# Optimization experiments

Measured on AMD Instinct MI355X. Metric: run time of the kernel, lower is better.

The kernel has to match this reference:

```python
import jax, jax.numpy as jnp
import numpy as np

N_ANCHORS = 262144
B = 4
G = 64
IM_SIZE = 1024.0
STRADDLE = 0.0
POS_THR = 0.5
NEG_THR = 0.3
FG_FRAC = 0.3
SAMPLE_BATCH = 512
TARGET_FG = int(FG_FRAC * SAMPLE_BATCH)  # 153
NEG_LOGIT = -1e9


def _jaccard(a, b):
    # Detectron-legacy '+1' box convention. a:[N,4], b:[G,4] -> [N,G]
    area_a = (a[:, 2] - a[:, 0] + 1.0) * (a[:, 3] - a[:, 1] + 1.0)
    area_b = (b[:, 2] - b[:, 0] + 1.0) * (b[:, 3] - b[:, 1] + 1.0)
    lt = jnp.maximum(a[:, None, :2], b[None, :, :2])
    rb = jnp.minimum(a[:, None, 2:], b[None, :, 2:])
    wh = jnp.clip(rb - lt + 1.0, 0.0)
    inter = wh[..., 0] * wh[..., 1]
    return inter / (area_a[:, None] + area_b[None, :] - inter)


def _bbox_transform_inv(ex, gt):
    ew = ex[:, 2] - ex[:, 0] + 1.0
    eh = ex[:, 3] - ex[:, 1] + 1.0
    ecx = ex[:, 0] + 0.5 * ew
    ecy = ex[:, 1] + 0.5 * eh
    gw = gt[:, 2] - gt[:, 0] + 1.0
    gh = gt[:, 3] - gt[:, 1] + 1.0
    gcx = gt[:, 0] + 0.5 * gw
    gcy = gt[:, 1] + 0.5 * gh
    return jnp.stack([(gcx - ecx) / ew, (gcy - ecy) / eh,
                      jnp.log(gw / ew), jnp.log(gh / eh)], axis=1)


def _match_single(boxes, gt_boxes, gt_ignore, im_info, key):
    # mask-based (jit-friendly) equivalent of forward_single_image; outside
    # anchors keep label -1 / targets 0, which reproduces the unmap() step.
    n = boxes.shape[0]
    im_h, im_w = im_info[0], im_info[1]
    inside = ((boxes[:, 0] >= -STRADDLE) & (boxes[:, 1] >= -STRADDLE)
              & (boxes[:, 2] < im_w + STRADDLE + 1.0)
              & (boxes[:, 3] < im_h + STRADDLE + 1.0))
    valid_gt = gt_ignore == 0  # gt_boxes[gt_ignore_labels == 0]
    iou = jnp.where(inside[:, None] & valid_gt[None, :], _jaccard(boxes, gt_boxes), 0.0)
    a2g_max = iou.max(axis=1)
    a2g_idx = iou.argmax(axis=1)
    g2a_max = iou.max(axis=0)
    g2a_max = jnp.where(g2a_max == 0.0, 1.0, g2a_max)  # avoid matching all-zero cols
    with_max = (iou == g2a_max[None, :]).any(axis=1)   # ensure_closest_box
    pos = inside & (with_max | (a2g_max >= POS_THR))
    labels = jnp.where(pos, 1, -1).astype(jnp.int32)
    # subsample positives down to TARGET_FG by random priority (keeps exactly
    # min(fg_num, TARGET_FG) positives, like the permutation-based disable)
    kp, kn = jax.random.split(key)
    prio = jnp.where(pos, jax.random.uniform(kp, (n,)), -jnp.inf)
    rank = jnp.argsort(jnp.argsort(-prio))
    labels = jnp.where(pos & (rank >= TARGET_FG), -1, labels)
    # sample negatives with replacement (torch.multinomial(..., replacement=True))
    num_fg = (labels > 0).sum()
    target_bg = SAMPLE_BATCH - num_fg
    neg = inside & (a2g_max < NEG_THR)
    do_sample = neg.sum() > target_bg
    samp = jax.random.categorical(kn, jnp.where(neg, 0.0, NEG_LOGIT), shape=(SAMPLE_BATCH,))
    valid_s = jnp.arange(SAMPLE_BATCH) < target_bg
    idx = jnp.where(valid_s, samp, n)  # invalid samples write to padded slot
    lab_ext = jnp.concatenate([labels, jnp.full((1,), -1, jnp.int32)])
    lab_samp = lab_ext.at[idx].set(0)[:n]
    labels = jnp.where(do_sample, lab_samp, labels)
    pos_final = labels > 0
    deltas = _bbox_transform_inv(boxes, gt_boxes[a2g_idx])
    bbox_targets = jnp.where(pos_final[:, None], deltas, 0.0)
    return labels, bbox_targets


def setup_inputs() -> dict:
    key = jax.random.key(0)
    k1, k2, k3, k4, k5, k6 = jax.random.split(key, 6)
    axy = jax.random.uniform(k1, (N_ANCHORS, 2), minval=-50.0, maxval=950.0)
    awh = jax.random.uniform(k2, (N_ANCHORS, 2), minval=16.0, maxval=160.0)
    boxes = jnp.concatenate([axy, axy + awh], axis=1)
    gxy = jax.random.uniform(k3, (B, G, 2), minval=0.0, maxval=800.0)
    gwh = jax.random.uniform(k4, (B, G, 2), minval=32.0, maxval=220.0)
    gt_boxes = jnp.concatenate([gxy, gxy + gwh], axis=2)
    gt_labels = jax.random.randint(k5, (B, G), 0, 80)
    gt_ignore_labels = jax.random.randint(k6, (B, G), 0, 2)
    im_info = jnp.tile(jnp.array([IM_SIZE, IM_SIZE, 1.0], jnp.float32), (B, 1))
    return {"boxes": boxes, "gt_boxes": gt_boxes, "gt_labels": gt_labels,
            "gt_ignore_labels": gt_ignore_labels, "im_info": im_info}


def reference(boxes, gt_boxes, gt_labels, gt_ignore_labels, im_info):
    # gt_labels is accepted but unused, exactly as in the torch module
    keys = jax.random.split(jax.random.key(42), gt_boxes.shape[0])
    labels, bbox_targets = jax.vmap(_match_single, in_axes=(None, 0, 0, 0, 0))(
        boxes.reshape(-1, 4), gt_boxes, gt_ignore_labels, im_info, keys)
    return labels, bbox_targets
```

## Files before the change

kernel.cpp:

```cpp
#include <hip/hip_runtime.h>
#include <stdint.h>

#define NANCH   262144
#define NB      4
#define NG      64
#define TGT_FG  153
#define SB      512
#define IDXMASK 262143u
#define NSH     8
#define SHCAP   (NANCH/NSH)

#define WS_PCNT     0
#define WS_G2A      4096
#define WS_KTH      5120
#define WS_TBG      5184
#define WS_DOSAMP   5248
#define WS_NUMPOS   5312
#define WS_SAMPKEY  8192
#define WS_ZERO_WORDS 6144
#define WS_A2G      32768
#define WS_NEG      (WS_A2G + NB*NANCH)
#define WS_POS      (WS_NEG + NB*NANCH*4)

#define PCNT_AT(pcnt, b, sh, L) ((pcnt)[(((b) * NSH + (sh)) * 2 + (L)) * 16])

struct RngKeys { uint32_t kp[NB][2]; uint32_t kn[NB][2]; };

#define TFR(r) { x0 += x1; x1 = (x1 << (r)) | (x1 >> (32 - (r))); x1 ^= x0; }
__host__ __device__ inline void tf2x32(uint32_t k0, uint32_t k1,
                                       uint32_t x0, uint32_t x1,
                                       uint32_t &o0, uint32_t &o1) {
  uint32_t k2 = k0 ^ k1 ^ 0x1BD11BDAu;
  x0 += k0; x1 += k1;
  TFR(13) TFR(15) TFR(26) TFR(6)   x0 += k1; x1 += k2 + 1u;
  TFR(17) TFR(29) TFR(16) TFR(24)  x0 += k2; x1 += k0 + 2u;
  TFR(13) TFR(15) TFR(26) TFR(6)   x0 += k0; x1 += k1 + 3u;
  TFR(17) TFR(29) TFR(16) TFR(24)  x0 += k1; x1 += k2 + 4u;
  TFR(13) TFR(15) TFR(26) TFR(6)   x0 += k2; x1 += k0 + 5u;
  o0 = x0; o1 = x1;
}

__host__ __device__ inline void tf_ctr(uint32_t k0, uint32_t k1, uint32_t i,
                                       uint32_t &o0, uint32_t &o1) {
  tf2x32(k0, k1, 0u, i, o0, o1);
}

__device__ __forceinline__ uint32_t draw_bits(uint32_t k0, uint32_t k1,
                                              uint32_t idx) {
  uint32_t o0, o1;
  tf_ctr(k0, k1, idx, o0, o1);
  return o0 ^ o1;
}

#define ROTL1(x, r) __builtin_amdgcn_alignbit((x), (x), 32 - (r))
#define TFQ(r) { x0 += x1; x1 = ROTL1(x1, r); x1 ^= x0; }
__device__ __forceinline__ uint32_t tf_bits_fast(uint32_t k0, uint32_t k1,
                                                 uint32_t k2, uint32_t x0,
                                                 uint32_t x1) {
  TFQ(13) TFQ(15) TFQ(26) TFQ(6)   x0 += k1; x1 += k2 + 1u;
  TFQ(17) TFQ(29) TFQ(16) TFQ(24)  x0 += k2; x1 += k0 + 2u;
  TFQ(13) TFQ(15) TFQ(26) TFQ(6)   x0 += k0; x1 += k1 + 3u;
  TFQ(17) TFQ(29) TFQ(16) TFQ(24)  x0 += k1; x1 += k2 + 4u;
  TFQ(13) TFQ(15) TFQ(26) TFQ(6)   x0 += k2; x1 += k0 + 5u;
  return x0 ^ x1;
}

__device__ __forceinline__ float box_area(float x1, float y1, float x2, float y2) {
#pragma clang fp contract(off)
  return ((x2 - x1) + 1.0f) * ((y2 - y1) + 1.0f);
}

__device__ __forceinline__ float iou_pair(float ax1, float ay1, float ax2, float ay2,
                                          float areaA, float gx1, float gy1,
                                          float gx2, float gy2, float areaB) {
#pragma clang fp contract(off)
  float ltx = fmaxf(ax1, gx1), lty = fmaxf(ay1, gy1);
  float rbx = fminf(ax2, gx2), rby = fminf(ay2, gy2);
  float w = fmaxf((rbx - ltx) + 1.0f, 0.0f);
  float h = fmaxf((rby - lty) + 1.0f, 0.0f);
  float inter = w * h;
  return inter / ((areaA + areaB) - inter);
}

__global__ __launch_bounds__(256) void k_init(unsigned int* w) {
  int i = blockIdx.x * 256 + threadIdx.x;
  if (i < WS_ZERO_WORDS) w[i] = 0u;
}

__global__ __launch_bounds__(256) void k_g2amax(
    const float4* __restrict__ boxes, const float4* __restrict__ gtb,
    const int* __restrict__ gti, const float* __restrict__ iminfo,
    unsigned int* __restrict__ g2a_u32) {
  int bx = blockIdx.x;
  int b = bx >> 8, chunk = bx & 255;
  int t = threadIdx.x, j = t & 63, sub = t >> 6;
  float4 g = gtb[b * NG + j];
  bool valid = (gti[b * NG + j] == 0);
  float areaB = box_area(g.x, g.y, g.z, g.w);
  float thrx = iminfo[b * 3 + 1] + 1.0f;
  float thry = iminfo[b * 3 + 0] + 1.0f;
  float m = 0.0f;
  int base = chunk * 1024 + sub * 256;
  #pragma unroll 2
  for (int i = 0; i < 256; ++i) {
    float4 bb = boxes[base + i];
    bool inside = (bb.x >= -0.0f) && (bb.y >= -0.0f) && (bb.z < thrx) && (bb.w < thry);
    float areaA = box_area(bb.x, bb.y, bb.z, bb.w);
    float v = iou_pair(bb.x, bb.y, bb.z, bb.w, areaA, g.x, g.y, g.z, g.w, areaB);
    v = (inside && valid) ? v : 0.0f;
    m = fmaxf(m, v);
  }
  __shared__ float red[4][64];
  red[sub][j] = m;
  __syncthreads();
  if (t < 64) {
    float mm = fmaxf(fmaxf(red[0][t], red[1][t]), fmaxf(red[2][t], red[3][t]));
    atomicMax(&g2a_u32[b * NG + t], __float_as_uint(mm));
  }
}

__global__ __launch_bounds__(256) void k_label(
    const float4* __restrict__ boxes, const float4* __restrict__ gtb,
    const int* __restrict__ gti, const float* __restrict__ iminfo,
    const float* __restrict__ g2a, float* __restrict__ labels,
    unsigned char* __restrict__ a2g, unsigned long long* __restrict__ pos_keys,
    unsigned int* __restrict__ neg_list, int* __restrict__ pcnt, RngKeys rk) {
  int bx = blockIdx.x;
  int b = bx >> 10, blk = bx & 1023;
  int t = threadIdx.x;
  int sh = blk & (NSH - 1);
  __shared__ float4 sg[NG];
  __shared__ float sab[NG], sval[NG], sadj[NG];
  if (t < NG) {
    float4 g = gtb[b * NG + t];
    sg[t] = g;
    sab[t] = box_area(g.x, g.y, g.z, g.w);
    sval[t] = (gti[b * NG + t] == 0) ? 1.0f : 0.0f;
    float gm = g2a[b * NG + t];
    sadj[t] = (gm == 0.0f) ? 1.0f : gm;
  }
  __syncthreads();
  int a = blk * 256 + t;
  float4 bb = boxes[a];
  float thrx = iminfo[b * 3 + 1] + 1.0f, thry = iminfo[b * 3 + 0] + 1.0f;
  bool inside = (bb.x >= -0.0f) && (bb.y >= -0.0f) && (bb.z < thrx) && (bb.w < thry);
  float areaA = box_area(bb.x, bb.y, bb.z, bb.w);
  float maxv = 0.0f; int amax = 0; bool wm = false;
  #pragma unroll 8
  for (int j = 0; j < NG; ++j) {
    float4 g = sg[j];
    float v = iou_pair(bb.x, bb.y, bb.z, bb.w, areaA, g.x, g.y, g.z, g.w, sab[j]);
    v = (inside && (sval[j] != 0.0f)) ? v : 0.0f;
    wm = wm || (v == sadj[j]);
    if (v > maxv) { maxv = v; amax = j; }
  }
  bool pos = inside && (wm || (maxv >= 0.5f));
  bool neg = inside && (maxv < 0.3f);
  labels[b * NANCH + a] = pos ? 1.0f : -1.0f;
  a2g[b * NANCH + a] = (unsigned char)amax;
  unsigned long long mpos = __ballot(pos);
  unsigned long long mneg = __ballot(neg);
  int lane = t & 63, wid = t >> 6;
  __shared__ int wc[4][2];
  __shared__ int bbase[2];
  if (lane == 0) { wc[wid][0] = __popcll(mpos); wc[wid][1] = __popcll(mneg); }
  __syncthreads();
  if (t == 0) {
    bbase[0] = atomicAdd(&PCNT_AT(pcnt, b, sh, 0),
                         wc[0][0] + wc[1][0] + wc[2][0] + wc[3][0]);
    bbase[1] = atomicAdd(&PCNT_AT(pcnt, b, sh, 1),
                         wc[0][1] + wc[1][1] + wc[2][1] + wc[3][1]);
  }
  __syncthreads();
  unsigned long long lt = (1ull << lane) - 1ull;
  if (pos) {
    int off = bbase[0] + __popcll(mpos & lt);
    for (int w = 0; w < wid; ++w) off += wc[w][0];
    uint32_t bits = draw_bits(rk.kp[b][0], rk.kp[b][1], (uint32_t)a);
    unsigned long long key =
        (((unsigned long long)(bits >> 9)) << 18) | (unsigned long long)(IDXMASK - (uint32_t)a);
    pos_keys[(size_t)b * NANCH + (size_t)sh * SHCAP + off] = key;
  }
  if (neg) {
    int off = bbase[1] + __popcll(mneg & lt);
    for (int w = 0; w < wid; ++w) off += wc[w][1];
    neg_list[(size_t)b * NANCH + (size_t)sh * SHCAP + off] = (unsigned int)a;
  }
}

__global__ __launch_bounds__(256) void k_select(
    const unsigned long long* __restrict__ pos_keys, const int* __restrict__ pcnt,
    unsigned long long* __restrict__ kth, int* __restrict__ tbg,
    int* __restrict__ dosamp, int* __restrict__ numpos) {
  int b = blockIdx.x, t = threadIdx.x;
  int scnt[NSH]; int np = 0, nn = 0;
  #pragma unroll
  for (int sh = 0; sh < NSH; ++sh) {
    scnt[sh] = PCNT_AT(pcnt, b, sh, 0);
    np += scnt[sh];
    nn += PCNT_AT(pcnt, b, sh, 1);
  }
  int nf = np < TGT_FG ? np : TGT_FG;
  int targ = SB - nf;
  if (t == 0) { tbg[b] = targ; dosamp[b] = (nn > targ) ? 1 : 0; numpos[b] = np; }
  if (np <= TGT_FG) { if (t == 0) kth[b] = 0ull; return; }
  __shared__ int cw[4];
  int lane = t & 63, wid = t >> 6;
  unsigned long long pref = 0ull;
  int r = TGT_FG;
  for (int bit = 40; bit >= 0; --bit) {
    unsigned long long cand = pref | (1ull << bit);
    unsigned long long mask = ~((1ull << bit) - 1ull);
    int c = 0;
    for (int sh = 0; sh < NSH; ++sh) {
      const unsigned long long* keys =
          pos_keys + (size_t)b * NANCH + (size_t)sh * SHCAP;
      for (int i = t; i < scnt[sh]; i += 256)
        c += ((keys[i] & mask) == cand) ? 1 : 0;
    }
    #pragma unroll
    for (int off = 32; off; off >>= 1) c += __shfl_xor(c, off, 64);
    __syncthreads();
    if (lane == 0) cw[wid] = c;
    __syncthreads();
    int total = cw[0] + cw[1] + cw[2] + cw[3];
    if (total >= r) pref = cand; else r -= total;
  }
  if (t == 0) kth[b] = pref;
}

__global__ __launch_bounds__(256) void k_disable(
    const unsigned long long* __restrict__ pos_keys, const int* __restrict__ pcnt,
    const int* __restrict__ numpos, const unsigned long long* __restrict__ kth,
    float* __restrict__ labels) {
  int b = blockIdx.x >> 6, blk = blockIdx.x & 63;
  if (numpos[b] <= TGT_FG) return;
  int sh = blk & (NSH - 1), sub = blk >> 3;
  int cnt = PCNT_AT(pcnt, b, sh, 0);
  unsigned long long K = kth[b];
  const unsigned long long* keys = pos_keys + (size_t)b * NANCH + (size_t)sh * SHCAP;
  for (int i = sub * 256 + threadIdx.x; i < cnt; i += 8 * 256) {
    unsigned long long key = keys[i];
    if (key < K) {
      int a = (int)(IDXMASK - (uint32_t)(key & (unsigned long long)IDXMASK));
      labels[b * NANCH + a] = -1.0f;
    }
  }
}

__global__ __launch_bounds__(256) void k_cat(
    const unsigned int* __restrict__ neg_list, const int* __restrict__ pcnt,
    const int* __restrict__ tbg, unsigned long long* __restrict__ samp_key,
    RngKeys rk) {
  int bx = blockIdx.x;
  int sh = bx & (NSH - 1);
  int pr = (bx >> 3) & 255;
  int b  = bx >> 11;
  int targ = tbg[b];
  int s0 = pr * 2;
  if (s0 >= targ) return;
  int nn = PCNT_AT(pcnt, b, sh, 1);
  uint32_t k0 = rk.kn[b][0], k1 = rk.kn[b][1];
  uint32_t k2 = k0 ^ k1 ^ 0x1BD11BDAu;
  uint32_t xb0 = ((uint32_t)s0 << 18) + k1;
  uint32_t xb1 = ((uint32_t)(s0 + 1) << 18) + k1;
  unsigned long long b0 = 0ull, b1 = 0ull;
  const unsigned int* nl = neg_list + (size_t)b * NANCH + (size_t)sh * SHCAP;
  int i = threadIdx.x;
  if (i < nn) {
    uint32_t a = nl[i];
    for (;;) {
      int inext = i + 256;
      bool has = inext < nn;
      uint32_t an = has ? nl[inext] : 0u;
      unsigned long long inv64 = (unsigned long long)(IDXMASK - a);
      { uint32_t bits = tf_bits_fast(k0, k1, k2, k0, xb0 + a);
        unsigned long long key = (((unsigned long long)(bits >> 9)) << 18) | inv64;
        if (key > b0) b0 = key; }
      { uint32_t bits = tf_bits_fast(k0, k1, k2, k0, xb1 + a);
        unsigned long long key = (((unsigned long long)(bits >> 9)) << 18) | inv64;
        if (key > b1) b1 = key; }
      if (!has) break;
      a = an; i = inext;
    }
  }
  #pragma unroll
  for (int off = 32; off; off >>= 1) {
    unsigned long long o0 = __shfl_xor(b0, off, 64); if (o0 > b0) b0 = o0;
    unsigned long long o1 = __shfl_xor(b1, off, 64); if (o1 > b1) b1 = o1;
  }
  __shared__ unsigned long long red[4][2];
  int lane = threadIdx.x & 63, wid = threadIdx.x >> 6;
  if (lane == 0) { red[wid][0] = b0; red[wid][1] = b1; }
  __syncthreads();
  if (threadIdx.x < 2) {
    int j = threadIdx.x;
    unsigned long long m = red[0][j];
    if (red[1][j] > m) m = red[1][j];
    if (red[2][j] > m) m = red[2][j];
    if (red[3][j] > m) m = red[3][j];
    if (s0 + j < targ) atomicMax(&samp_key[b * SB + s0 + j], m);
  }
}

__global__ __launch_bounds__(256) void k_scatter(
    const unsigned long long* __restrict__ samp_key, const int* __restrict__ tbg,
    const int* __restrict__ dosamp, float* __restrict__ labels) {
  int b = blockIdx.x >> 1;
  int s = ((blockIdx.x & 1) << 8) | threadIdx.x;
  if (!dosamp[b]) return;
  if (s < tbg[b]) {
    unsigned long long key = samp_key[b * SB + s];
    int a = (int)(IDXMASK - (uint32_t)(key & (unsigned long long)IDXMASK));
    labels[b * NANCH + a] = 0.0f;
  }
}

__global__ __launch_bounds__(256) void k_targets(
    const float4* __restrict__ boxes, const float4* __restrict__ gtb,
    const unsigned char* __restrict__ a2g, const float* __restrict__ labels,
    float4* __restrict__ tout) {
  int bx = blockIdx.x;
  int b = bx >> 10, blk = bx & 1023;
  int a = blk * 256 + threadIdx.x;
  float lab = labels[b * NANCH + a];
  float4 o = make_float4(0.f, 0.f, 0.f, 0.f);
  if (lab > 0.0f) {
    float4 e = boxes[a];
    float4 g = gtb[b * NG + a2g[b * NANCH + a]];
    float ew = e.z - e.x + 1.0f, eh = e.w - e.y + 1.0f;
    float ecx = e.x + 0.5f * ew, ecy = e.y + 0.5f * eh;
    float gw = g.z - g.x + 1.0f, gh = g.w - g.y + 1.0f;
    float gcx = g.x + 0.5f * gw, gcy = g.y + 0.5f * gh;
    o.x = (gcx - ecx) / ew;
    o.y = (gcy - ecy) / eh;
    o.z = logf(gw / ew);
    o.w = logf(gh / eh);
  }
  tout[(size_t)b * NANCH + a] = o;
}

extern "C" void kernel_launch(void* const* d_in, const int* in_sizes, int n_in,
                              void* d_out, int out_size, void* d_ws, size_t ws_size,
                              hipStream_t stream) {
  const float4* boxes  = (const float4*)d_in[0];
  const float4* gtb    = (const float4*)d_in[1];
  const int*    gti    = (const int*)d_in[3];
  const float*  iminfo = (const float*)d_in[4];
  float*  labels = (float*)d_out;
  float4* tout   = (float4*)(labels + (size_t)NB * NANCH);

  char* wsb = (char*)d_ws;
  int*                pcnt     = (int*)(wsb + WS_PCNT);
  unsigned int*       g2a_u32  = (unsigned int*)(wsb + WS_G2A);
  float*              g2a_f    = (float*)(wsb + WS_G2A);
  unsigned long long* kth      = (unsigned long long*)(wsb + WS_KTH);
  int*                tbg      = (int*)(wsb + WS_TBG);
  int*                dosamp   = (int*)(wsb + WS_DOSAMP);
  int*                numpos   = (int*)(wsb + WS_NUMPOS);
  unsigned long long* samp_key = (unsigned long long*)(wsb + WS_SAMPKEY);
  unsigned char*      a2g      = (unsigned char*)(wsb + WS_A2G);
  unsigned int*       neg_list = (unsigned int*)(wsb + WS_NEG);
  unsigned long long* pos_keys = (unsigned long long*)(wsb + WS_POS);

  RngKeys rk;
  for (int b = 0; b < NB; ++b) {
    uint32_t a0, a1;
    tf_ctr(0u, 42u, (uint32_t)b, a0, a1);
    tf_ctr(a0, a1, 0u, rk.kp[b][0], rk.kp[b][1]);
    tf_ctr(a0, a1, 1u, rk.kn[b][0], rk.kn[b][1]);
  }

  k_init   <<<24, 256, 0, stream>>>((unsigned int*)wsb);
  k_g2amax <<<NB * (NANCH / 1024), 256, 0, stream>>>(boxes, gtb, gti, iminfo, g2a_u32);
  k_label  <<<NB * (NANCH / 256), 256, 0, stream>>>(boxes, gtb, gti, iminfo, g2a_f,
                                                    labels, a2g, pos_keys, neg_list,
                                                    pcnt, rk);
  k_select <<<NB, 256, 0, stream>>>(pos_keys, pcnt, kth, tbg, dosamp, numpos);
  k_disable<<<NB * 64, 256, 0, stream>>>(pos_keys, pcnt, numpos, kth, labels);
  k_cat    <<<NB * 256 * NSH, 256, 0, stream>>>(neg_list, pcnt, tbg, samp_key, rk);
  k_scatter<<<NB * 2, 256, 0, stream>>>(samp_key, tbg, dosamp, labels);
  k_targets<<<NB * (NANCH / 256), 256, 0, stream>>>(boxes, gtb, a2g, labels, tout);
}
```

Before: 891.6 us.

## Replace bitwise radix select with histogram bucket select; drop g2a atomics

The k-th key selection for positive subsampling used to scan all positive keys in global memory 41 times, once per bit. It now builds a 4096-bin shared-memory histogram of the top key bits and locates the bucket holding the 153rd largest key. It gathers that bucket's keys into shared memory and runs the bitwise refinement on only those, falling back to global scans if the bucket overflows. Separately, the per-GT max IoU reduction writes per-chunk partial maxima and reduces them in a new small kernel instead of using float atomicMax, at the cost of one extra launch.

```diff
diff --git a/kernel.cpp b/kernel.cpp
--- a/kernel.cpp
+++ b/kernel.cpp
@@ -11,14 +11,15 @@
 #define SHCAP   (NANCH/NSH)
 
 #define WS_PCNT     0
-#define WS_G2A      4096
-#define WS_KTH      5120
-#define WS_TBG      5184
-#define WS_DOSAMP   5248
-#define WS_NUMPOS   5312
+#define WS_KTH      4096
+#define WS_TBG      4160
+#define WS_DOSAMP   4224
+#define WS_NUMPOS   4288
+#define WS_G2A      4352
 #define WS_SAMPKEY  8192
 #define WS_ZERO_WORDS 6144
-#define WS_A2G      32768
+#define WS_GMAXC    32768
+#define WS_A2G      294912
 #define WS_NEG      (WS_A2G + NB*NANCH)
 #define WS_POS      (WS_NEG + NB*NANCH*4)
 
@@ -90,7 +91,7 @@
 __global__ __launch_bounds__(256) void k_g2amax(
     const float4* __restrict__ boxes, const float4* __restrict__ gtb,
     const int* __restrict__ gti, const float* __restrict__ iminfo,
-    unsigned int* __restrict__ g2a_u32) {
+    float* __restrict__ gmaxc) {
   int bx = blockIdx.x;
   int b = bx >> 8, chunk = bx & 255;
   int t = threadIdx.x, j = t & 63, sub = t >> 6;
@@ -115,8 +116,23 @@
   __syncthreads();
   if (t < 64) {
     float mm = fmaxf(fmaxf(red[0][t], red[1][t]), fmaxf(red[2][t], red[3][t]));
-    atomicMax(&g2a_u32[b * NG + t], __float_as_uint(mm));
-  }
+    gmaxc[((b << 8) + chunk) * 64 + t] = mm;
+  }
+}
+
+__global__ __launch_bounds__(256) void k_g2afin(
+    const float* __restrict__ gmaxc, float* __restrict__ g2a) {
+  int b = blockIdx.x, t = threadIdx.x;
+  int j = t & 63, part = t >> 6;
+  float m = 0.0f;
+  for (int c = part * 64; c < part * 64 + 64; ++c)
+    m = fmaxf(m, gmaxc[((b << 8) + c) * 64 + j]);
+  __shared__ float red[4][64];
+  red[part][j] = m;
+  __syncthreads();
+  if (t < 64)
+    g2a[b * NG + t] = fmaxf(fmaxf(red[0][t], red[1][t]),
+                            fmaxf(red[2][t], red[3][t]));
 }
 
 __global__ __launch_bounds__(256) void k_label(
@@ -188,11 +204,14 @@
   }
 }
 
+#define HB   4096
+#define BCAP 3072
 __global__ __launch_bounds__(256) void k_select(
     const unsigned long long* __restrict__ pos_keys, const int* __restrict__ pcnt,
     unsigned long long* __restrict__ kth, int* __restrict__ tbg,
     int* __restrict__ dosamp, int* __restrict__ numpos) {
   int b = blockIdx.x, t = threadIdx.x;
+  int lane = t & 63, wid = t >> 6;
   int scnt[NSH]; int np = 0, nn = 0;
   #pragma unroll
   for (int sh = 0; sh < NSH; ++sh) {
@@ -204,29 +223,97 @@
   int targ = SB - nf;
   if (t == 0) { tbg[b] = targ; dosamp[b] = (nn > targ) ? 1 : 0; numpos[b] = np; }
   if (np <= TGT_FG) { if (t == 0) kth[b] = 0ull; return; }
-  __shared__ int cw[4];
-  int lane = t & 63, wid = t >> 6;
-  unsigned long long pref = 0ull;
-  int r = TGT_FG;
-  for (int bit = 40; bit >= 0; --bit) {
-    unsigned long long cand = pref | (1ull << bit);
-    unsigned long long mask = ~((1ull << bit) - 1ull);
-    int c = 0;
-    for (int sh = 0; sh < NSH; ++sh) {
-      const unsigned long long* keys =
-          pos_keys + (size_t)b * NANCH + (size_t)sh * SHCAP;
-      for (int i = t; i < scnt[sh]; i += 256)
-        c += ((keys[i] & mask) == cand) ? 1 : 0;
-    }
-    #pragma unroll
-    for (int off = 32; off; off >>= 1) c += __shfl_xor(c, off, 64);
-    __syncthreads();
-    if (lane == 0) cw[wid] = c;
-    __syncthreads();
-    int total = cw[0] + cw[1] + cw[2] + cw[3];
-    if (total >= r) pref = cand; else r -= total;
-  }
-  if (t == 0) kth[b] = pref;
+
+  __shared__ unsigned int hist[HB];
+  __shared__ unsigned int part[256];
+  __shared__ unsigned long long buf[BCAP];
+  __shared__ int bufcnt, bucketB, rprime, cw[4];
+  for (int i = t; i < HB; i += 256) hist[i] = 0u;
+  if (t == 0) { bufcnt = 0; bucketB = -1; }
+  __syncthreads();
+  for (int sh = 0; sh < NSH; ++sh) {
+    const unsigned long long* keys = pos_keys + (size_t)b * NANCH + (size_t)sh * SHCAP;
+    for (int i = t; i < scnt[sh]; i += 256)
+      atomicAdd(&hist[(unsigned int)(keys[i] >> 29)], 1u);
+  }
+  __syncthreads();
+  unsigned int S = 0;
+  #pragma unroll
+  for (int k = 0; k < 16; ++k) S += hist[t * 16 + k];
+  part[t] = S;
+  __syncthreads();
+  if (t == 0) {
+    unsigned int run = 0;
+    for (int i = 255; i >= 0; --i) { unsigned int p = part[i]; part[i] = run; run += p; }
+  }
+  __syncthreads();
+  {
+    unsigned int above = part[t];
+    for (int k = 15; k >= 0; --k) {
+      unsigned int h = hist[t * 16 + k];
+      if (above < TGT_FG && above + h >= TGT_FG) {
+        bucketB = t * 16 + k; rprime = TGT_FG - (int)above;
+      }
+      above += h;
+    }
+  }
+  __syncthreads();
+  int B = bucketB, rp = rprime;
+  for (int sh = 0; sh < NSH; ++sh) {
+    const unsigned long long* keys = pos_keys + (size_t)b * NANCH + (size_t)sh * SHCAP;
+    for (int i = t; i < scnt[sh]; i += 256) {
+      unsigned long long key = keys[i];
+      if ((int)(key >> 29) == B) {
+        int p = atomicAdd(&bufcnt, 1);
+        if (p < BCAP) buf[p] = key;
+      }
+    }
+  }
+  __syncthreads();
+  int cnt = bufcnt;
+  unsigned int pref = 0u; int r = rp;
+  if (cnt <= BCAP) {
+    for (int bit = 28; bit >= 0; --bit) {
+      unsigned int cand = pref | (1u << bit);
+      unsigned int mask = (~((1u << bit) - 1u)) & 0x1FFFFFFFu;
+      int c = 0;
+      for (int i = t; i < cnt; i += 256) {
+        unsigned int low = (unsigned int)(buf[i] & 0x1FFFFFFFull);
+        c += ((low & mask) == cand) ? 1 : 0;
+      }
+      #pragma unroll
+      for (int off = 32; off; off >>= 1) c += __shfl_xor(c, off, 64);
+      if (lane == 0) cw[wid] = c;
+      __syncthreads();
+      int total = cw[0] + cw[1] + cw[2] + cw[3];
+      if (total >= r) pref = cand; else r -= total;
+      __syncthreads();
+    }
+  } else {
+    for (int bit = 28; bit >= 0; --bit) {
+      unsigned int cand = pref | (1u << bit);
+      unsigned int mask = (~((1u << bit) - 1u)) & 0x1FFFFFFFu;
+      int c = 0;
+      for (int sh = 0; sh < NSH; ++sh) {
+        const unsigned long long* keys = pos_keys + (size_t)b * NANCH + (size_t)sh * SHCAP;
+        for (int i = t; i < scnt[sh]; i += 256) {
+          unsigned long long key = keys[i];
+          if ((int)(key >> 29) == B) {
+            unsigned int low = (unsigned int)(key & 0x1FFFFFFFull);
+            c += ((low & mask) == cand) ? 1 : 0;
+          }
+        }
+      }
+      #pragma unroll
+      for (int off = 32; off; off >>= 1) c += __shfl_xor(c, off, 64);
+      if (lane == 0) cw[wid] = c;
+      __syncthreads();
+      int total = cw[0] + cw[1] + cw[2] + cw[3];
+      if (total >= r) pref = cand; else r -= total;
+      __syncthreads();
+    }
+  }
+  if (t == 0) kth[b] = (((unsigned long long)B) << 29) | (unsigned long long)pref;
 }
 
 __global__ __launch_bounds__(256) void k_disable(
@@ -352,13 +439,13 @@
 
   char* wsb = (char*)d_ws;
   int*                pcnt     = (int*)(wsb + WS_PCNT);
-  unsigned int*       g2a_u32  = (unsigned int*)(wsb + WS_G2A);
-  float*              g2a_f    = (float*)(wsb + WS_G2A);
   unsigned long long* kth      = (unsigned long long*)(wsb + WS_KTH);
   int*                tbg      = (int*)(wsb + WS_TBG);
   int*                dosamp   = (int*)(wsb + WS_DOSAMP);
   int*                numpos   = (int*)(wsb + WS_NUMPOS);
+  float*              g2a_f    = (float*)(wsb + WS_G2A);
   unsigned long long* samp_key = (unsigned long long*)(wsb + WS_SAMPKEY);
+  float*              gmaxc    = (float*)(wsb + WS_GMAXC);
   unsigned char*      a2g      = (unsigned char*)(wsb + WS_A2G);
   unsigned int*       neg_list = (unsigned int*)(wsb + WS_NEG);
   unsigned long long* pos_keys = (unsigned long long*)(wsb + WS_POS);
@@ -372,7 +459,8 @@
   }
 
   k_init   <<<24, 256, 0, stream>>>((unsigned int*)wsb);
-  k_g2amax <<<NB * (NANCH / 1024), 256, 0, stream>>>(boxes, gtb, gti, iminfo, g2a_u32);
+  k_g2amax <<<NB * (NANCH / 1024), 256, 0, stream>>>(boxes, gtb, gti, iminfo, gmaxc);
+  k_g2afin <<<NB, 256, 0, stream>>>(gmaxc, g2a_f);
   k_label  <<<NB * (NANCH / 256), 256, 0, stream>>>(boxes, gtb, gti, iminfo, g2a_f,
                                                     labels, a2g, pos_keys, neg_list,
                                                     pcnt, rk);
```

Result: faster. 785.1 us (-11.9%).

## Merge select into negative-sampling kernel and replace g2a atomics with two-pass reduction

Applied to the files above, without the earlier changes.

The per-image k-th positive radix select and the negative sampling kernel now run in one launch. The first NB blocks do the select and the remaining blocks do the negative draws, so the serial select overlaps the sampling work. The global per-GT maximum now goes through a per-chunk buffer plus a small finalize kernel instead of float atomicMax. The init kernel becomes a hipMemsetAsync, and the negative list is read as uint4 vectors. This trades an extra launch and workspace buffer for less atomic contention and less serialization, though the merged select blocks may become a long tail.

```diff
diff --git a/kernel.cpp b/kernel.cpp
--- a/kernel.cpp
+++ b/kernel.cpp
@@ -11,14 +11,15 @@
 #define SHCAP   (NANCH/NSH)
 
 #define WS_PCNT     0
-#define WS_G2A      4096
-#define WS_KTH      5120
-#define WS_TBG      5184
-#define WS_DOSAMP   5248
-#define WS_NUMPOS   5312
+#define WS_KTH      4096
+#define WS_TBG      4160
+#define WS_DOSAMP   4224
+#define WS_NUMPOS   4288
+#define WS_G2A      4352
 #define WS_SAMPKEY  8192
-#define WS_ZERO_WORDS 6144
-#define WS_A2G      32768
+#define WS_ZERO_BYTES 24576
+#define WS_GMAXC    32768
+#define WS_A2G      294912
 #define WS_NEG      (WS_A2G + NB*NANCH)
 #define WS_POS      (WS_NEG + NB*NANCH*4)
 
@@ -82,15 +83,10 @@
   return inter / ((areaA + areaB) - inter);
 }
 
-__global__ __launch_bounds__(256) void k_init(unsigned int* w) {
-  int i = blockIdx.x * 256 + threadIdx.x;
-  if (i < WS_ZERO_WORDS) w[i] = 0u;
-}
-
 __global__ __launch_bounds__(256) void k_g2amax(
     const float4* __restrict__ boxes, const float4* __restrict__ gtb,
     const int* __restrict__ gti, const float* __restrict__ iminfo,
-    unsigned int* __restrict__ g2a_u32) {
+    float* __restrict__ gmaxc) {
   int bx = blockIdx.x;
   int b = bx >> 8, chunk = bx & 255;
   int t = threadIdx.x, j = t & 63, sub = t >> 6;
@@ -115,8 +111,23 @@
   __syncthreads();
   if (t < 64) {
     float mm = fmaxf(fmaxf(red[0][t], red[1][t]), fmaxf(red[2][t], red[3][t]));
-    atomicMax(&g2a_u32[b * NG + t], __float_as_uint(mm));
-  }
+    gmaxc[((b << 8) + chunk) * 64 + t] = mm;
+  }
+}
+
+__global__ __launch_bounds__(256) void k_g2afin(
+    const float* __restrict__ gmaxc, float* __restrict__ g2a) {
+  int b = blockIdx.x, t = threadIdx.x;
+  int j = t & 63, part = t >> 6;
+  float m = 0.0f;
+  for (int c = part * 64; c < part * 64 + 64; ++c)
+    m = fmaxf(m, gmaxc[((b << 8) + c) * 64 + j]);
+  __shared__ float red[4][64];
+  red[part][j] = m;
+  __syncthreads();
+  if (t < 64)
+    g2a[b * NG + t] = fmaxf(fmaxf(red[0][t], red[1][t]),
+                            fmaxf(red[2][t], red[3][t]));
 }
 
 __global__ __launch_bounds__(256) void k_label(
@@ -188,45 +199,102 @@
   }
 }
 
-__global__ __launch_bounds__(256) void k_select(
-    const unsigned long long* __restrict__ pos_keys, const int* __restrict__ pcnt,
+__global__ __launch_bounds__(256) void k_catsel(
+    const unsigned int* __restrict__ neg_list,
+    const unsigned long long* __restrict__ pos_keys,
+    const int* __restrict__ pcnt, unsigned long long* __restrict__ samp_key,
     unsigned long long* __restrict__ kth, int* __restrict__ tbg,
-    int* __restrict__ dosamp, int* __restrict__ numpos) {
-  int b = blockIdx.x, t = threadIdx.x;
-  int scnt[NSH]; int np = 0, nn = 0;
+    int* __restrict__ dosamp, int* __restrict__ numpos, RngKeys rk) {
+  int bx = blockIdx.x;
+  int t = threadIdx.x, lane = t & 63, wid = t >> 6;
+
+  if (bx < NB) {
+    int b = bx;
+    __shared__ int cw[4];
+    int scnt[NSH]; int np = 0, nnb = 0;
+    #pragma unroll
+    for (int sh = 0; sh < NSH; ++sh) {
+      scnt[sh] = PCNT_AT(pcnt, b, sh, 0);
+      np += scnt[sh];
+      nnb += PCNT_AT(pcnt, b, sh, 1);
+    }
+    int nf = np < TGT_FG ? np : TGT_FG;
+    int targ = SB - nf;
+    if (t == 0) { tbg[b] = targ; dosamp[b] = (nnb > targ) ? 1 : 0; numpos[b] = np; }
+    if (np <= TGT_FG) { if (t == 0) kth[b] = 0ull; return; }
+    unsigned long long pref = 0ull;
+    int r = TGT_FG;
+    for (int bit = 40; bit >= 0; --bit) {
+      unsigned long long cand = pref | (1ull << bit);
+      unsigned long long mask = ~((1ull << bit) - 1ull);
+      int c = 0;
+      for (int sh = 0; sh < NSH; ++sh) {
+        const unsigned long long* keys =
+            pos_keys + (size_t)b * NANCH + (size_t)sh * SHCAP;
+        for (int i = t; i < scnt[sh]; i += 256)
+          c += ((keys[i] & mask) == cand) ? 1 : 0;
+      }
+      #pragma unroll
+      for (int off = 32; off; off >>= 1) c += __shfl_xor(c, off, 64);
+      __syncthreads();
+      if (lane == 0) cw[wid] = c;
+      __syncthreads();
+      int total = cw[0] + cw[1] + cw[2] + cw[3];
+      if (total >= r) pref = cand; else r -= total;
+    }
+    if (t == 0) kth[b] = pref;
+    return;
+  }
+
+  int bx2 = bx - NB;
+  int sh = bx2 & (NSH - 1);
+  int pr = (bx2 >> 3) & 255;
+  int b  = bx2 >> 11;
+  int np = 0;
   #pragma unroll
-  for (int sh = 0; sh < NSH; ++sh) {
-    scnt[sh] = PCNT_AT(pcnt, b, sh, 0);
-    np += scnt[sh];
-    nn += PCNT_AT(pcnt, b, sh, 1);
-  }
-  int nf = np < TGT_FG ? np : TGT_FG;
-  int targ = SB - nf;
-  if (t == 0) { tbg[b] = targ; dosamp[b] = (nn > targ) ? 1 : 0; numpos[b] = np; }
-  if (np <= TGT_FG) { if (t == 0) kth[b] = 0ull; return; }
-  __shared__ int cw[4];
-  int lane = t & 63, wid = t >> 6;
-  unsigned long long pref = 0ull;
-  int r = TGT_FG;
-  for (int bit = 40; bit >= 0; --bit) {
-    unsigned long long cand = pref | (1ull << bit);
-    unsigned long long mask = ~((1ull << bit) - 1ull);
-    int c = 0;
-    for (int sh = 0; sh < NSH; ++sh) {
-      const unsigned long long* keys =
-          pos_keys + (size_t)b * NANCH + (size_t)sh * SHCAP;
-      for (int i = t; i < scnt[sh]; i += 256)
-        c += ((keys[i] & mask) == cand) ? 1 : 0;
-    }
-    #pragma unroll
-    for (int off = 32; off; off >>= 1) c += __shfl_xor(c, off, 64);
-    __syncthreads();
-    if (lane == 0) cw[wid] = c;
-    __syncthreads();
-    int total = cw[0] + cw[1] + cw[2] + cw[3];
-    if (total >= r) pref = cand; else r -= total;
-  }
-  if (t == 0) kth[b] = pref;
+  for (int s = 0; s < NSH; ++s) np += PCNT_AT(pcnt, b, s, 0);
+  int targ = SB - (np < TGT_FG ? np : TGT_FG);
+  int s0 = pr * 2;
+  if (s0 >= targ) return;
+  int nn = PCNT_AT(pcnt, b, sh, 1);
+  uint32_t k0 = rk.kn[b][0], k1 = rk.kn[b][1];
+  uint32_t k2 = k0 ^ k1 ^ 0x1BD11BDAu;
+  uint32_t xb0 = ((uint32_t)s0 << 18) + k1;
+  uint32_t xb1 = ((uint32_t)(s0 + 1) << 18) + k1;
+  unsigned long long b0 = 0ull, b1 = 0ull;
+  const unsigned int* nl = neg_list + (size_t)b * NANCH + (size_t)sh * SHCAP;
+#define PROC1(A) { uint32_t a_ = (A); \
+    unsigned long long inv64 = (unsigned long long)(IDXMASK - a_); \
+    { uint32_t bits = tf_bits_fast(k0, k1, k2, k0, xb0 + a_); \
+      unsigned long long key = (((unsigned long long)(bits >> 9)) << 18) | inv64; \
+      if (key > b0) b0 = key; } \
+    { uint32_t bits = tf_bits_fast(k0, k1, k2, k0, xb1 + a_); \
+      unsigned long long key = (((unsigned long long)(bits >> 9)) << 18) | inv64; \
+      if (key > b1) b1 = key; } }
+  int nv = nn >> 2;
+  const uint4* nl4 = (const uint4*)nl;
+  for (int iv = t; iv < nv; iv += 256) {
+    uint4 q = nl4[iv];
+    PROC1(q.x) PROC1(q.y) PROC1(q.z) PROC1(q.w)
+  }
+  for (int i = (nv << 2) + t; i < nn; i += 256) { PROC1(nl[i]) }
+#undef PROC1
+  #pragma unroll
+  for (int off = 32; off; off >>= 1) {
+    unsigned long long o0 = __shfl_xor(b0, off, 64); if (o0 > b0) b0 = o0;
+    unsigned long long o1 = __shfl_xor(b1, off, 64); if (o1 > b1) b1 = o1;
+  }
+  __shared__ unsigned long long red[4][2];
+  if (lane == 0) { red[wid][0] = b0; red[wid][1] = b1; }
+  __syncthreads();
+  if (t < 2) {
+    int j = t;
+    unsigned long long m = red[0][j];
+    if (red[1][j] > m) m = red[1][j];
+    if (red[2][j] > m) m = red[2][j];
+    if (red[3][j] > m) m = red[3][j];
+    if (s0 + j < targ) atomicMax(&samp_key[b * SB + s0 + j], m);
+  }
 }
 
 __global__ __launch_bounds__(256) void k_disable(
@@ -245,61 +313,6 @@
       int a = (int)(IDXMASK - (uint32_t)(key & (unsigned long long)IDXMASK));
       labels[b * NANCH + a] = -1.0f;
     }
-  }
-}
-
-__global__ __launch_bounds__(256) void k_cat(
-    const unsigned int* __restrict__ neg_list, const int* __restrict__ pcnt,
-    const int* __restrict__ tbg, unsigned long long* __restrict__ samp_key,
-    RngKeys rk) {
-  int bx = blockIdx.x;
-  int sh = bx & (NSH - 1);
-  int pr = (bx >> 3) & 255;
-  int b  = bx >> 11;
-  int targ = tbg[b];
-  int s0 = pr * 2;
-  if (s0 >= targ) return;
-  int nn = PCNT_AT(pcnt, b, sh, 1);
-  uint32_t k0 = rk.kn[b][0], k1 = rk.kn[b][1];
-  uint32_t k2 = k0 ^ k1 ^ 0x1BD11BDAu;
-  uint32_t xb0 = ((uint32_t)s0 << 18) + k1;
-  uint32_t xb1 = ((uint32_t)(s0 + 1) << 18) + k1;
-  unsigned long long b0 = 0ull, b1 = 0ull;
-  const unsigned int* nl = neg_list + (size_t)b * NANCH + (size_t)sh * SHCAP;
-  int i = threadIdx.x;
-  if (i < nn) {
-    uint32_t a = nl[i];
-    for (;;) {
-      int inext = i + 256;
-      bool has = inext < nn;
-      uint32_t an = has ? nl[inext] : 0u;
-      unsigned long long inv64 = (unsigned long long)(IDXMASK - a);
-      { uint32_t bits = tf_bits_fast(k0, k1, k2, k0, xb0 + a);
-        unsigned long long key = (((unsigned long long)(bits >> 9)) << 18) | inv64;
-        if (key > b0) b0 = key; }
-      { uint32_t bits = tf_bits_fast(k0, k1, k2, k0, xb1 + a);
-        unsigned long long key = (((unsigned long long)(bits >> 9)) << 18) | inv64;
-        if (key > b1) b1 = key; }
-      if (!has) break;
-      a = an; i = inext;
-    }
-  }
-  #pragma unroll
-  for (int off = 32; off; off >>= 1) {
-    unsigned long long o0 = __shfl_xor(b0, off, 64); if (o0 > b0) b0 = o0;
-    unsigned long long o1 = __shfl_xor(b1, off, 64); if (o1 > b1) b1 = o1;
-  }
-  __shared__ unsigned long long red[4][2];
-  int lane = threadIdx.x & 63, wid = threadIdx.x >> 6;
-  if (lane == 0) { red[wid][0] = b0; red[wid][1] = b1; }
-  __syncthreads();
-  if (threadIdx.x < 2) {
-    int j = threadIdx.x;
-    unsigned long long m = red[0][j];
-    if (red[1][j] > m) m = red[1][j];
-    if (red[2][j] > m) m = red[2][j];
-    if (red[3][j] > m) m = red[3][j];
-    if (s0 + j < targ) atomicMax(&samp_key[b * SB + s0 + j], m);
   }
 }
 
@@ -352,13 +365,13 @@
 
   char* wsb = (char*)d_ws;
   int*                pcnt     = (int*)(wsb + WS_PCNT);
-  unsigned int*       g2a_u32  = (unsigned int*)(wsb + WS_G2A);
-  float*              g2a_f    = (float*)(wsb + WS_G2A);
   unsigned long long* kth      = (unsigned long long*)(wsb + WS_KTH);
   int*                tbg      = (int*)(wsb + WS_TBG);
   int*                dosamp   = (int*)(wsb + WS_DOSAMP);
   int*                numpos   = (int*)(wsb + WS_NUMPOS);
+  float*              g2a_f    = (float*)(wsb + WS_G2A);
   unsigned long long* samp_key = (unsigned long long*)(wsb + WS_SAMPKEY);
+  float*              gmaxc    = (float*)(wsb + WS_GMAXC);
   unsigned char*      a2g      = (unsigned char*)(wsb + WS_A2G);
   unsigned int*       neg_list = (unsigned int*)(wsb + WS_NEG);
   unsigned long long* pos_keys = (unsigned long long*)(wsb + WS_POS);
@@ -371,14 +384,16 @@
     tf_ctr(a0, a1, 1u, rk.kn[b][0], rk.kn[b][1]);
   }
 
-  k_init   <<<24, 256, 0, stream>>>((unsigned int*)wsb);
-  k_g2amax <<<NB * (NANCH / 1024), 256, 0, stream>>>(boxes, gtb, gti, iminfo, g2a_u32);
+  hipMemsetAsync(wsb, 0, WS_ZERO_BYTES, stream);
+  k_g2amax <<<NB * (NANCH / 1024), 256, 0, stream>>>(boxes, gtb, gti, iminfo, gmaxc);
+  k_g2afin <<<NB, 256, 0, stream>>>(gmaxc, g2a_f);
   k_label  <<<NB * (NANCH / 256), 256, 0, stream>>>(boxes, gtb, gti, iminfo, g2a_f,
                                                     labels, a2g, pos_keys, neg_list,
                                                     pcnt, rk);
-  k_select <<<NB, 256, 0, stream>>>(pos_keys, pcnt, kth, tbg, dosamp, numpos);
+  k_catsel <<<NB + NB * 256 * NSH, 256, 0, stream>>>(neg_list, pos_keys, pcnt,
+                                                     samp_key, kth, tbg, dosamp,
+                                                     numpos, rk);
   k_disable<<<NB * 64, 256, 0, stream>>>(pos_keys, pcnt, numpos, kth, labels);
-  k_cat    <<<NB * 256 * NSH, 256, 0, stream>>>(neg_list, pcnt, tbg, samp_key, rk);
   k_scatter<<<NB * 2, 256, 0, stream>>>(samp_key, tbg, dosamp, labels);
   k_targets<<<NB * (NANCH / 256), 256, 0, stream>>>(boxes, gtb, a2g, labels, tout);
 }
```

Result: faster. 745.7 us (-16.4%).
